# Performance work log

Measured on AMD Instinct MI355X. Metric: run time of the kernel, lower is better.

The kernel has to match this reference:

```python
import jax, jax.numpy as jnp
import numpy as np

B, S, H, E, V = 256, 512, 512, 128, 30000
RNN_IN = H + E + 1  # weighted context + id embedding + rate


def setup_inputs() -> dict:
    key = jax.random.key(0)
    ks = jax.random.split(key, 16)
    nrm = lambda k, shape, s=0.02: jax.random.normal(k, shape, dtype=jnp.float32) * s
    return {
        "input_id": jax.random.randint(ks[0], (B, 1), 0, V),
        "input_rate": jax.random.uniform(ks[1], (B, 1), dtype=jnp.float32),
        "hidden": nrm(ks[2], (1, B, H), 1.0),
        "encoder_outputs": nrm(ks[3], (S, B, H), 1.0),
        "attn_mask": jax.random.randint(ks[4], (B, S), 0, 2),
        "constraint_vec": (jax.random.uniform(ks[5], (B, V)) > 0.3).astype(jnp.float32),
        "emb_id": nrm(ks[6], (V, E)),
        "attn_w": nrm(ks[7], (2 * H, H)),
        "attn_b": jnp.zeros((H,), jnp.float32),
        "v_w": nrm(ks[8], (H,)),
        "w_ih": nrm(ks[9], (3 * H, RNN_IN)),
        "w_hh": nrm(ks[10], (3 * H, H)),
        "b_ih": jnp.zeros((3 * H,), jnp.float32),
        "b_hh": jnp.zeros((3 * H,), jnp.float32),
        "fc_id_w": nrm(ks[11], (H, V)),
        "fc_id_b": jnp.zeros((V,), jnp.float32),
        "tandem_w": nrm(ks[12], (E + H, H)),
        "tandem_b": jnp.zeros((H,), jnp.float32),
        "rate_w": nrm(ks[13], (H, 1)),
        "rate_b": jnp.zeros((1,), jnp.float32),
    }


def reference(input_id, input_rate, hidden, encoder_outputs, attn_mask,
              constraint_vec, emb_id, attn_w, attn_b, v_w,
              w_ih, w_hh, b_ih, b_hh, fc_id_w, fc_id_b,
              tandem_w, tandem_b, rate_w, rate_b):
    hd = hidden.shape[-1]
    h0 = hidden[0]                                # [B, H]
    embedded = emb_id[input_id[:, 0]]             # [B, E] (dropout p=0 -> identity)

    # --- additive attention (concat-linear split to avoid [B,S,2H] concat) ---
    enc = jnp.transpose(encoder_outputs, (1, 0, 2))         # [B, S, H]
    hid_part = h0 @ attn_w[:hd]                             # [B, H]
    enc_part = jnp.einsum('bsh,hk->bsk', enc, attn_w[hd:])  # [B, S, H]
    energy = jnp.tanh(hid_part[:, None, :] + enc_part + attn_b)
    scores = jnp.einsum('bsh,h->bs', energy, v_w)           # [B, S]
    scores = jnp.where(attn_mask == 0, jnp.float32(-1e10), scores)
    a = jax.nn.softmax(scores, axis=1)
    weighted = jnp.einsum('bs,bsh->bh', a, enc)             # [B, H]

    # --- GRU cell (torch gate order: r, z, n) ---
    x = jnp.concatenate([weighted, embedded, input_rate], axis=1)  # [B, H+E+1]
    gi = x @ w_ih.T + b_ih
    gh = h0 @ w_hh.T + b_hh
    gi_r, gi_z, gi_n = jnp.split(gi, 3, axis=1)
    gh_r, gh_z, gh_n = jnp.split(gh, 3, axis=1)
    r = jax.nn.sigmoid(gi_r + gh_r)
    z = jax.nn.sigmoid(gi_z + gh_z)
    n = jnp.tanh(gi_n + r * gh_n)
    h1 = (1.0 - z) * n + z * h0                   # [B, H]

    # --- masked log-softmax over id vocabulary ---
    logits = h1 @ fc_id_w + fc_id_b               # [B, V]
    maxes = jnp.max(logits, axis=1, keepdims=True)
    x_exp = jnp.exp(logits - maxes) * constraint_vec
    pred = jnp.clip(x_exp / jnp.sum(x_exp, axis=1, keepdims=True), 1e-6, 1.0)
    prediction_id = jnp.log(pred)

    # --- tandem rate head ---
    max_id = jnp.argmax(prediction_id, axis=1)
    id_emb = emb_id[max_id]                       # [B, E]
    rate_in = jax.nn.relu(jnp.concatenate([id_emb, h1], axis=1) @ tandem_w + tandem_b)
    prediction_rate = jax.nn.sigmoid(rate_in @ rate_w + rate_b)  # [B, 1]

    return prediction_id, prediction_rate, h1[None]  # hidden [1, B, H]
```

## Files before the change

### kernel.cpp

```cpp
#include <hip/hip_runtime.h>
#include <hip/hip_bf16.h>

#define B_ 256
#define S_ 512
#define H_ 512
#define E_ 128
#define V_ 30000
#define RNNIN_ 641

using bf16x8 = __attribute__((ext_vector_type(8))) short;
using f32x4  = __attribute__((ext_vector_type(4))) float;

__device__ __forceinline__ short f2bf(float f) {
  unsigned int u = __float_as_uint(f);
  u += 0x7fffu + ((u >> 16) & 1u);
  return (short)(u >> 16);
}

__device__ __forceinline__ float fast_tanh(float x) {
  x = fminf(10.f, fmaxf(-10.f, x));
  float t = __expf(2.f * x);
  return (t - 1.f) / (t + 1.f);
}

__device__ __forceinline__ float sigmoidf(float x) {
  return 1.f / (1.f + __expf(-x));
}

__global__ __launch_bounds__(256) void transpose_cvt(
    const float* __restrict__ in, unsigned short* __restrict__ out, int K, int N)
{
  __shared__ unsigned short tile[32][33];
  int n0 = blockIdx.x * 32, k0 = blockIdx.y * 32;
  int tx = threadIdx.x, ty = threadIdx.y;
  #pragma unroll
  for (int i = 0; i < 4; i++) {
    int k = k0 + ty + i * 8, n = n0 + tx;
    float v = (k < K && n < N) ? in[(size_t)k * N + n] : 0.f;
    tile[ty + i * 8][tx] = (unsigned short)f2bf(v);
  }
  __syncthreads();
  #pragma unroll
  for (int i = 0; i < 4; i++) {
    int n = n0 + ty + i * 8, k = k0 + tx;
    if (n < N && k < K) out[(size_t)n * K + k] = tile[tx][ty + i * 8];
  }
}

template<bool BT, bool RELU>
__global__ __launch_bounds__(256) void gemm_f32(
    const float* __restrict__ A, const float* __restrict__ Bm,
    const float* __restrict__ bias, float* __restrict__ C,
    int M, int N, int K)
{
  __shared__ float As[16][65];
  __shared__ float Bs[16][65];
  const int m0 = blockIdx.x * 64, n0 = blockIdx.y * 64;
  const int tid = threadIdx.x;
  const int tx = tid & 15, ty = tid >> 4;
  float acc[4][4] = {};
  for (int k0 = 0; k0 < K; k0 += 16) {
    __syncthreads();
    #pragma unroll
    for (int i = 0; i < 4; i++) {
      int e = tid + i * 256;
      int m = e >> 4, k = e & 15;
      float v = 0.f;
      if (m0 + m < M && k0 + k < K) v = A[(size_t)(m0 + m) * K + k0 + k];
      As[k][m] = v;
    }
    #pragma unroll
    for (int i = 0; i < 4; i++) {
      int e = tid + i * 256;
      if (BT) {
        int n = e >> 4, k = e & 15;
        float v = 0.f;
        if (n0 + n < N && k0 + k < K) v = Bm[(size_t)(n0 + n) * K + k0 + k];
        Bs[k][n] = v;
      } else {
        int k = e >> 6, n = e & 63;
        float v = 0.f;
        if (n0 + n < N && k0 + k < K) v = Bm[(size_t)(k0 + k) * N + n0 + n];
        Bs[k][n] = v;
      }
    }
    __syncthreads();
    #pragma unroll
    for (int k = 0; k < 16; k++) {
      float a[4], b[4];
      #pragma unroll
      for (int i = 0; i < 4; i++) a[i] = As[k][ty * 4 + i];
      #pragma unroll
      for (int j = 0; j < 4; j++) b[j] = Bs[k][tx * 4 + j];
      #pragma unroll
      for (int i = 0; i < 4; i++)
        #pragma unroll
        for (int j = 0; j < 4; j++) acc[i][j] += a[i] * b[j];
    }
  }
  #pragma unroll
  for (int i = 0; i < 4; i++) {
    int m = m0 + ty * 4 + i;
    if (m >= M) continue;
    #pragma unroll
    for (int j = 0; j < 4; j++) {
      int n = n0 + tx * 4 + j;
      if (n >= N) continue;
      float v = acc[i][j] + (bias ? bias[n] : 0.f);
      if (RELU) v = fmaxf(v, 0.f);
      C[(size_t)m * N + n] = v;
    }
  }
}

__global__ __launch_bounds__(512, 4) void attn_gemm_score(
    const float* __restrict__ A, const unsigned short* __restrict__ Bt,
    const float* __restrict__ hid_pb, const float* __restrict__ v_w,
    float* __restrict__ scores)
{
  __shared__ short As[4 * 64 * 8];
  __shared__ short Bs[8 * 4 * 64 * 8];
  const int m0 = blockIdx.x * 64;
  const int tid = threadIdx.x;
  const int lane = tid & 63;
  const int wv = tid >> 6;
  const int quad = lane >> 4, l15 = lane & 15;

  f32x4 acc[4][4];
  #pragma unroll
  for (int i = 0; i < 4; i++)
    #pragma unroll
    for (int j = 0; j < 4; j++) acc[i][j] = f32x4{0.f, 0.f, 0.f, 0.f};

  for (int kt = 0; kt < 16; kt++) {
    const int kb = kt * 32;
    __syncthreads();
    if (tid < 256) {
      int m = tid >> 2, q = tid & 3;
      const float* src = A + (size_t)(m0 + m) * H_ + kb + q * 8;
      float4 v0 = *(const float4*)src;
      float4 v1 = *(const float4*)(src + 4);
      bf16x8 pk;
      pk[0] = f2bf(v0.x); pk[1] = f2bf(v0.y); pk[2] = f2bf(v0.z); pk[3] = f2bf(v0.w);
      pk[4] = f2bf(v1.x); pk[5] = f2bf(v1.y); pk[6] = f2bf(v1.z); pk[7] = f2bf(v1.w);
      int ti = m >> 4, ld = q * 16 + (m & 15);
      *(bf16x8*)&As[(ti * 64 + ld) * 8] = pk;
    }
    #pragma unroll
    for (int p = 0; p < 4; p++) {
      int n = p * 128 + (tid >> 2), q = tid & 3;
      bf16x8 v = *(const bf16x8*)(Bt + (size_t)n * H_ + kb + q * 8);
      int wvd = n >> 6, tj = (n >> 4) & 3, ld = q * 16 + (n & 15);
      *(bf16x8*)&Bs[((wvd * 4 + tj) * 64 + ld) * 8] = v;
    }
    __syncthreads();
    bf16x8 a[4], b[4];
    #pragma unroll
    for (int ti = 0; ti < 4; ti++) a[ti] = *(const bf16x8*)&As[(ti * 64 + lane) * 8];
    #pragma unroll
    for (int tj = 0; tj < 4; tj++) b[tj] = *(const bf16x8*)&Bs[((wv * 4 + tj) * 64 + lane) * 8];
    #pragma unroll
    for (int ti = 0; ti < 4; ti++)
      #pragma unroll
      for (int tj = 0; tj < 4; tj++)
        acc[ti][tj] = __builtin_amdgcn_mfma_f32_16x16x32_bf16(a[ti], b[tj], acc[ti][tj], 0, 0, 0);
  }

  #pragma unroll
  for (int ti = 0; ti < 4; ti++) {
    #pragma unroll
    for (int r = 0; r < 4; r++) {
      int m = m0 + ti * 16 + quad * 4 + r;
      int b = m & (B_ - 1);
      int s = m >> 8;
      float sum = 0.f;
      #pragma unroll
      for (int tj = 0; tj < 4; tj++) {
        int n = wv * 64 + tj * 16 + l15;
        float v = acc[ti][tj][r] + hid_pb[b * H_ + n];
        sum += fast_tanh(v) * v_w[n];
      }
      sum += __shfl_xor(sum, 1);
      sum += __shfl_xor(sum, 2);
      sum += __shfl_xor(sum, 4);
      sum += __shfl_xor(sum, 8);
      if (l15 == 0) atomicAdd(scores + b * S_ + s, sum);
    }
  }
}

__global__ __launch_bounds__(256, 4) void logits_gemm(
    const unsigned short* __restrict__ Ab, const float* __restrict__ Bw,
    const float* __restrict__ bias, float* __restrict__ C)
{
  __shared__ short As[2 * 16 * 64 * 8];
  __shared__ short Bs[2 * 4 * 64 * 8];
  const int n0 = blockIdx.x * 64;
  const int tid = threadIdx.x;
  const int lane = tid & 63;
  const int wv = tid >> 6;
  const int quad = lane >> 4, l15 = lane & 15;

  f32x4 acc[4][4];
  #pragma unroll
  for (int i = 0; i < 4; i++)
    #pragma unroll
    for (int j = 0; j < 4; j++) acc[i][j] = f32x4{0.f, 0.f, 0.f, 0.f};

  const int nB  = tid & 63;
  const int kg  = tid >> 6;
  const int cB  = kg >> 1;
  const int q0  = (kg & 1) * 2;
  const int tjB = nB >> 4;
  const bool nOK = (n0 + nB) < V_;

  for (int kt = 0; kt < 8; kt++) {
    const int kb = kt * 64;
    __syncthreads();
    #pragma unroll
    for (int p = 0; p < 8; p++) {
      int m = p * 32 + (tid >> 3), f = tid & 7;
      int c = f >> 2, q = f & 3;
      bf16x8 v = *(const bf16x8*)(Ab + (size_t)m * H_ + kb + c * 32 + q * 8);
      int mt = m >> 4, ld = q * 16 + (m & 15);
      *(bf16x8*)&As[((c * 16 + mt) * 64 + ld) * 8] = v;
    }
    {
      float col[16];
      const float* src = Bw + (size_t)(kb + kg * 16) * V_ + n0 + nB;
      #pragma unroll
      for (int i = 0; i < 16; i++) col[i] = nOK ? src[(size_t)i * V_] : 0.f;
      bf16x8 f0, f1;
      #pragma unroll
      for (int i = 0; i < 8; i++) { f0[i] = f2bf(col[i]); f1[i] = f2bf(col[8 + i]); }
      int ld0 = q0 * 16 + (nB & 15);
      *(bf16x8*)&Bs[((cB * 4 + tjB) * 64 + ld0) * 8] = f0;
      *(bf16x8*)&Bs[((cB * 4 + tjB) * 64 + ld0 + 16) * 8] = f1;
    }
    __syncthreads();
    #pragma unroll
    for (int c = 0; c < 2; c++) {
      bf16x8 a[4], b[4];
      #pragma unroll
      for (int ti = 0; ti < 4; ti++)
        a[ti] = *(const bf16x8*)&As[((c * 16 + wv * 4 + ti) * 64 + lane) * 8];
      #pragma unroll
      for (int tj = 0; tj < 4; tj++)
        b[tj] = *(const bf16x8*)&Bs[((c * 4 + tj) * 64 + lane) * 8];
      #pragma unroll
      for (int ti = 0; ti < 4; ti++)
        #pragma unroll
        for (int tj = 0; tj < 4; tj++)
          acc[ti][tj] = __builtin_amdgcn_mfma_f32_16x16x32_bf16(a[ti], b[tj], acc[ti][tj], 0, 0, 0);
    }
  }
  #pragma unroll
  for (int ti = 0; ti < 4; ti++)
    #pragma unroll
    for (int r = 0; r < 4; r++) {
      int m = wv * 64 + ti * 16 + quad * 4 + r;
      #pragma unroll
      for (int tj = 0; tj < 4; tj++) {
        int n = n0 + tj * 16 + l15;
        if (n < V_) C[(size_t)m * V_ + n] = acc[ti][tj][r] + bias[n];
      }
    }
}

__global__ __launch_bounds__(256) void attn_softmax(
    const float* __restrict__ scores, const int* __restrict__ mask, float* __restrict__ aw)
{
  int b = blockIdx.x, tid = threadIdx.x;
  __shared__ float red[256];
  float v0 = scores[b * S_ + tid];
  float v1 = scores[b * S_ + tid + 256];
  if (mask[b * S_ + tid] == 0) v0 = -1e10f;
  if (mask[b * S_ + tid + 256] == 0) v1 = -1e10f;
  red[tid] = fmaxf(v0, v1);
  __syncthreads();
  for (int off = 128; off; off >>= 1) { if (tid < off) red[tid] = fmaxf(red[tid], red[tid + off]); __syncthreads(); }
  float mx = red[0];
  __syncthreads();
  float e0 = __expf(v0 - mx), e1 = __expf(v1 - mx);
  red[tid] = e0 + e1;
  __syncthreads();
  for (int off = 128; off; off >>= 1) { if (tid < off) red[tid] += red[tid + off]; __syncthreads(); }
  float inv = 1.f / red[0];
  aw[b * S_ + tid] = e0 * inv;
  aw[b * S_ + tid + 256] = e1 * inv;
}

__global__ __launch_bounds__(512) void attn_weighted(
    const float* __restrict__ aw, const float* __restrict__ enc, float* __restrict__ weighted)
{
  int b = blockIdx.x, h = threadIdx.x;
  __shared__ float a_s[S_];
  a_s[h] = aw[b * S_ + h];
  __syncthreads();
  float acc = 0.f;
  #pragma unroll 8
  for (int s = 0; s < S_; s++)
    acc += a_s[s] * enc[((size_t)s * B_ + b) * H_ + h];
  weighted[b * H_ + h] = acc;
}

__global__ void build_x(const float* __restrict__ weighted, const int* __restrict__ ids,
                        const float* __restrict__ emb, const float* __restrict__ rate,
                        float* __restrict__ x)
{
  int i = blockIdx.x * 256 + threadIdx.x;
  if (i >= B_ * RNNIN_) return;
  int b = i / RNNIN_, j = i % RNNIN_;
  float v;
  if (j < H_) v = weighted[b * H_ + j];
  else if (j < H_ + E_) v = emb[(size_t)ids[b] * E_ + (j - H_)];
  else v = rate[b];
  x[i] = v;
}

__global__ void gru_gates(const float* __restrict__ gi, const float* __restrict__ gh,
                          const float* __restrict__ h0, float* __restrict__ h1,
                          unsigned short* __restrict__ h1b, float* __restrict__ h1_out)
{
  int i = blockIdx.x * 256 + threadIdx.x;
  int b = i >> 9, j = i & (H_ - 1);
  const float* gib = gi + (size_t)b * 1536;
  const float* ghb = gh + (size_t)b * 1536;
  float r = sigmoidf(gib[j] + ghb[j]);
  float z = sigmoidf(gib[512 + j] + ghb[512 + j]);
  float n = fast_tanh(gib[1024 + j] + r * ghb[1024 + j]);
  float h = (1.f - z) * n + z * h0[i];
  h1[i] = h;
  h1b[i] = (unsigned short)f2bf(h);
  h1_out[i] = h;
}

__global__ __launch_bounds__(1024) void softmax_fused(
    float* __restrict__ lp, const float* __restrict__ cv, int* __restrict__ maxid)
{
  int b = blockIdx.x, tid = threadIdx.x;
  int wid = tid >> 6, lane = tid & 63;
  float* row = lp + (size_t)b * V_;
  const float* cvr = cv + (size_t)b * V_;
  __shared__ float redf[16];
  __shared__ float rede[16];
  __shared__ int   redi[16];

  float mx = -INFINITY;
  for (int v = tid; v < V_; v += 1024) mx = fmaxf(mx, row[v]);
  #pragma unroll
  for (int o = 1; o < 64; o <<= 1) mx = fmaxf(mx, __shfl_xor(mx, o));
  if (lane == 0) redf[wid] = mx;
  __syncthreads();
  if (tid == 0) {
    float m = redf[0];
    for (int i = 1; i < 16; i++) m = fmaxf(m, redf[i]);
    redf[0] = m;
  }
  __syncthreads();
  float M = redf[0];
  __syncthreads();

  float s = 0.f, best = -1.f;
  int bi = 0;
  for (int v = tid; v < V_; v += 1024) {
    float e = __expf(row[v] - M) * cvr[v];
    row[v] = e;
    s += e;
    if (e > best) { best = e; bi = v; }
  }
  #pragma unroll
  for (int o = 1; o < 64; o <<= 1) {
    s += __shfl_xor(s, o);
    float ob = __shfl_xor(best, o);
    int oi = __shfl_xor(bi, o);
    if (ob > best || (ob == best && oi < bi)) { best = ob; bi = oi; }
  }
  if (lane == 0) { redf[wid] = s; rede[wid] = best; redi[wid] = bi; }
  __syncthreads();
  if (tid == 0) {
    float ss = 0.f, bb = rede[0];
    int ii = redi[0];
    for (int i = 0; i < 16; i++) {
      ss += redf[i];
      if (rede[i] > bb || (rede[i] == bb && redi[i] < ii)) { bb = rede[i]; ii = redi[i]; }
    }
    redf[0] = ss;
    maxid[b] = ii;
  }
  __syncthreads();
  float inv = 1.f / redf[0];
  for (int v = tid; v < V_; v += 1024) {
    float p = row[v] * inv;
    p = fminf(fmaxf(p, 1e-6f), 1.f);
    row[v] = __logf(p);
  }
}

__global__ void build_tandem(const int* __restrict__ maxid, const float* __restrict__ emb,
                             const float* __restrict__ h1, float* __restrict__ t)
{
  int i = blockIdx.x * 256 + threadIdx.x;
  if (i >= B_ * 640) return;
  int b = i / 640, j = i % 640;
  t[i] = (j < E_) ? emb[(size_t)maxid[b] * E_ + j] : h1[b * H_ + (j - E_)];
}

__global__ __launch_bounds__(64) void rate_head(const float* __restrict__ rate_in,
                                                const float* __restrict__ rate_w,
                                                const float* __restrict__ rate_b,
                                                float* __restrict__ out)
{
  int b = blockIdx.x, t = threadIdx.x;
  float s = 0.f;
  #pragma unroll
  for (int i = 0; i < 8; i++) s += rate_in[b * H_ + t + 64 * i] * rate_w[t + 64 * i];
  #pragma unroll
  for (int m = 32; m; m >>= 1) s += __shfl_xor(s, m);
  if (t == 0) out[b] = sigmoidf(s + rate_b[0]);
}

extern "C" void kernel_launch(void* const* d_in, const int* in_sizes, int n_in,
                              void* d_out, int out_size, void* d_ws, size_t ws_size,
                              hipStream_t stream)
{
  const int*   input_id   = (const int*)  d_in[0];
  const float* input_rate = (const float*)d_in[1];
  const float* hidden     = (const float*)d_in[2];
  const float* enc        = (const float*)d_in[3];
  const int*   attn_mask  = (const int*)  d_in[4];
  const float* cv         = (const float*)d_in[5];
  const float* emb        = (const float*)d_in[6];
  const float* attn_w     = (const float*)d_in[7];
  const float* attn_b     = (const float*)d_in[8];
  const float* v_w        = (const float*)d_in[9];
  const float* w_ih       = (const float*)d_in[10];
  const float* w_hh       = (const float*)d_in[11];
  const float* b_ih       = (const float*)d_in[12];
  const float* b_hh       = (const float*)d_in[13];
  const float* fc_w       = (const float*)d_in[14];
  const float* fc_b       = (const float*)d_in[15];
  const float* tan_w      = (const float*)d_in[16];
  const float* tan_b      = (const float*)d_in[17];
  const float* rate_w     = (const float*)d_in[18];
  const float* rate_b     = (const float*)d_in[19];

  float* out = (float*)d_out;
  float* ws  = (float*)d_ws;
  float* hid_pb   = ws;
  float* scores   = ws + 131072;
  float* aw       = ws + 262144;
  float* weighted = ws + 393216;
  float* xbuf     = ws + 524288;
  float* gi       = ws + 688384;
  float* gh       = ws + 1081600;
  float* h1       = ws + 1474816;
  float* rate_in  = ws + 1605888;
  int*   maxid    = (int*)(ws + 1736960);
  unsigned short* Bt  = (unsigned short*)(ws + 1737216);
  unsigned short* h1b = (unsigned short*)(ws + 1868288);

  float* out_pred = out;
  float* out_rate = out + (size_t)B_ * V_;
  float* out_h1   = out + (size_t)B_ * V_ + B_;

  transpose_cvt<<<dim3(16, 16), dim3(32, 8), 0, stream>>>(attn_w + (size_t)H_ * H_, Bt, H_, H_);

  hipMemsetAsync(scores, 0, (size_t)B_ * S_ * sizeof(float), stream);

  gemm_f32<false, false><<<dim3(4, 8), 256, 0, stream>>>(hidden, attn_w, attn_b, hid_pb, B_, H_, H_);

  attn_gemm_score<<<2048, 512, 0, stream>>>(enc, Bt, hid_pb, v_w, scores);

  attn_softmax<<<B_, 256, 0, stream>>>(scores, attn_mask, aw);
  attn_weighted<<<B_, 512, 0, stream>>>(aw, enc, weighted);
  build_x<<<641, 256, 0, stream>>>(weighted, input_id, emb, input_rate, xbuf);

  gemm_f32<true, false><<<dim3(4, 24), 256, 0, stream>>>(xbuf, w_ih, b_ih, gi, B_, 1536, RNNIN_);
  gemm_f32<true, false><<<dim3(4, 24), 256, 0, stream>>>(hidden, w_hh, b_hh, gh, B_, 1536, H_);
  gru_gates<<<512, 256, 0, stream>>>(gi, gh, hidden, h1, h1b, out_h1);

  logits_gemm<<<469, 256, 0, stream>>>(h1b, fc_w, fc_b, out_pred);
  softmax_fused<<<B_, 1024, 0, stream>>>(out_pred, cv, maxid);

  build_tandem<<<640, 256, 0, stream>>>(maxid, emb, h1, xbuf);
  gemm_f32<false, true><<<dim3(4, 8), 256, 0, stream>>>(xbuf, tan_w, tan_b, rate_in, B_, H_, 640);
  rate_head<<<B_, 64, 0, stream>>>(rate_in, rate_w, rate_b, out_rate);
}
```

Before: 1.177 ms.

## Restructure attention score GEMM with direct-to-LDS B loads and register prefetch

Result: faster. 1.042 ms (-11.5%).

```diff
diff --git a/kernel.cpp b/kernel.cpp
--- a/kernel.cpp
+++ b/kernel.cpp
@@ -27,24 +27,20 @@
   return 1.f / (1.f + __expf(-x));
 }
 
-__global__ __launch_bounds__(256) void transpose_cvt(
-    const float* __restrict__ in, unsigned short* __restrict__ out, int K, int N)
-{
-  __shared__ unsigned short tile[32][33];
-  int n0 = blockIdx.x * 32, k0 = blockIdx.y * 32;
-  int tx = threadIdx.x, ty = threadIdx.y;
-  #pragma unroll
-  for (int i = 0; i < 4; i++) {
-    int k = k0 + ty + i * 8, n = n0 + tx;
-    float v = (k < K && n < N) ? in[(size_t)k * N + n] : 0.f;
-    tile[ty + i * 8][tx] = (unsigned short)f2bf(v);
-  }
-  __syncthreads();
-  #pragma unroll
-  for (int i = 0; i < 4; i++) {
-    int n = n0 + ty + i * 8, k = k0 + tx;
-    if (n < N && k < K) out[(size_t)n * K + k] = tile[tx][ty + i * 8];
-  }
+__device__ __forceinline__ void gload_lds16(const void* g, void* l) {
+  __builtin_amdgcn_global_load_lds(
+      (const __attribute__((address_space(1))) void*)g,
+      (__attribute__((address_space(3))) void*)l, 16, 0, 0);
+}
+
+__global__ __launch_bounds__(256) void pack_b(
+    const float* __restrict__ in, unsigned short* __restrict__ out)
+{
+  int i = blockIdx.x * 256 + threadIdx.x;
+  int k = i >> 9, n = i & 511;
+  float v = in[i];
+  int idx = ((((k >> 5) * 32 + (n >> 4)) * 4 + ((k >> 3) & 3)) * 16 + (n & 15)) * 8 + (k & 7);
+  out[idx] = (unsigned short)f2bf(v);
 }
 
 template<bool BT, bool RELU>
@@ -113,70 +109,171 @@
   }
 }
 
-__global__ __launch_bounds__(512, 4) void attn_gemm_score(
-    const float* __restrict__ A, const unsigned short* __restrict__ Bt,
+__device__ void gemm_bt_dev(float (*As)[65], float (*Bs)[65],
+    const float* __restrict__ A, const float* __restrict__ Bm,
+    const float* __restrict__ bias, float* __restrict__ C,
+    int M, int N, int K)
+{
+  const int m0 = blockIdx.x * 64, n0 = blockIdx.y * 64;
+  const int tid = threadIdx.x;
+  const int tx = tid & 15, ty = tid >> 4;
+  float acc[4][4] = {};
+  for (int k0 = 0; k0 < K; k0 += 16) {
+    __syncthreads();
+    #pragma unroll
+    for (int i = 0; i < 4; i++) {
+      int e = tid + i * 256;
+      int m = e >> 4, k = e & 15;
+      float v = 0.f;
+      if (m0 + m < M && k0 + k < K) v = A[(size_t)(m0 + m) * K + k0 + k];
+      As[k][m] = v;
+    }
+    #pragma unroll
+    for (int i = 0; i < 4; i++) {
+      int e = tid + i * 256;
+      int n = e >> 4, k = e & 15;
+      float v = 0.f;
+      if (n0 + n < N && k0 + k < K) v = Bm[(size_t)(n0 + n) * K + k0 + k];
+      Bs[k][n] = v;
+    }
+    __syncthreads();
+    #pragma unroll
+    for (int k = 0; k < 16; k++) {
+      float a[4], b[4];
+      #pragma unroll
+      for (int i = 0; i < 4; i++) a[i] = As[k][ty * 4 + i];
+      #pragma unroll
+      for (int j = 0; j < 4; j++) b[j] = Bs[k][tx * 4 + j];
+      #pragma unroll
+      for (int i = 0; i < 4; i++)
+        #pragma unroll
+        for (int j = 0; j < 4; j++) acc[i][j] += a[i] * b[j];
+    }
+  }
+  #pragma unroll
+  for (int i = 0; i < 4; i++) {
+    int m = m0 + ty * 4 + i;
+    if (m >= M) continue;
+    #pragma unroll
+    for (int j = 0; j < 4; j++) {
+      int n = n0 + tx * 4 + j;
+      if (n >= N) continue;
+      C[(size_t)m * N + n] = acc[i][j] + bias[n];
+    }
+  }
+}
+
+__global__ __launch_bounds__(256) void gemm_gru(
+    const float* __restrict__ xb, const float* __restrict__ w_ih,
+    const float* __restrict__ b_ih, float* __restrict__ gi,
+    const float* __restrict__ hid, const float* __restrict__ w_hh,
+    const float* __restrict__ b_hh, float* __restrict__ gh)
+{
+  __shared__ float As[16][65];
+  __shared__ float Bs[16][65];
+  if (blockIdx.z == 0) gemm_bt_dev(As, Bs, xb, w_ih, b_ih, gi, B_, 1536, RNNIN_);
+  else                 gemm_bt_dev(As, Bs, hid, w_hh, b_hh, gh, B_, 1536, H_);
+}
+
+__global__ __launch_bounds__(256, 3) void attn_gemm_score(
+    const float* __restrict__ A, const unsigned short* __restrict__ Btf,
     const float* __restrict__ hid_pb, const float* __restrict__ v_w,
     float* __restrict__ scores)
 {
-  __shared__ short As[4 * 64 * 8];
-  __shared__ short Bs[8 * 4 * 64 * 8];
-  const int m0 = blockIdx.x * 64;
-  const int tid = threadIdx.x;
+  __shared__ short As[2 * 4 * 64 * 8];
+  __shared__ short Bs[2 * 16 * 64 * 8];
+
+  const int bid  = blockIdx.x;
+  const int tile = (bid & 7) * 512 + (bid >> 3);
+  const int mblk = tile >> 1, nblk = tile & 1;
+  const int m0 = mblk * 64, n0 = nblk * 256;
+
+  const int tid  = threadIdx.x;
   const int lane = tid & 63;
-  const int wv = tid >> 6;
+  const int wv   = tid >> 6;
   const int quad = lane >> 4, l15 = lane & 15;
 
+  const int arow = tid >> 2;
+  const int aseg = tid & 3;
+  const float* aptr = A + (size_t)(m0 + arow) * H_ + aseg * 16;
+  const int ac = aseg >> 1, aq0 = (aseg & 1) * 2;
+  short* aw0 = &As[((ac * 4 + (arow >> 4)) * 64 + aq0 * 16 + (arow & 15)) * 8];
+  short* aw1 = aw0 + 16 * 8;
+
+  const unsigned short* bsrc = Btf + nblk * 8192;
+
   f32x4 acc[4][4];
   #pragma unroll
   for (int i = 0; i < 4; i++)
     #pragma unroll
     for (int j = 0; j < 4; j++) acc[i][j] = f32x4{0.f, 0.f, 0.f, 0.f};
 
-  for (int kt = 0; kt < 16; kt++) {
-    const int kb = kt * 32;
-    __syncthreads();
-    if (tid < 256) {
-      int m = tid >> 2, q = tid & 3;
-      const float* src = A + (size_t)(m0 + m) * H_ + kb + q * 8;
-      float4 v0 = *(const float4*)src;
-      float4 v1 = *(const float4*)(src + 4);
-      bf16x8 pk;
-      pk[0] = f2bf(v0.x); pk[1] = f2bf(v0.y); pk[2] = f2bf(v0.z); pk[3] = f2bf(v0.w);
-      pk[4] = f2bf(v1.x); pk[5] = f2bf(v1.y); pk[6] = f2bf(v1.z); pk[7] = f2bf(v1.w);
-      int ti = m >> 4, ld = q * 16 + (m & 15);
-      *(bf16x8*)&As[(ti * 64 + ld) * 8] = pk;
-    }
-    #pragma unroll
-    for (int p = 0; p < 4; p++) {
-      int n = p * 128 + (tid >> 2), q = tid & 3;
-      bf16x8 v = *(const bf16x8*)(Bt + (size_t)n * H_ + kb + q * 8);
-      int wvd = n >> 6, tj = (n >> 4) & 3, ld = q * 16 + (n & 15);
-      *(bf16x8*)&Bs[((wvd * 4 + tj) * 64 + ld) * 8] = v;
-    }
-    __syncthreads();
-    bf16x8 a[4], b[4];
-    #pragma unroll
-    for (int ti = 0; ti < 4; ti++) a[ti] = *(const bf16x8*)&As[(ti * 64 + lane) * 8];
-    #pragma unroll
-    for (int tj = 0; tj < 4; tj++) b[tj] = *(const bf16x8*)&Bs[((wv * 4 + tj) * 64 + lane) * 8];
-    #pragma unroll
-    for (int ti = 0; ti < 4; ti++)
+  float4 rA[4];
+  #pragma unroll
+  for (int i = 0; i < 4; i++) rA[i] = *(const float4*)(aptr + i * 4);
+
+  for (int kt = 0; kt < 8; kt++) {
+    __builtin_amdgcn_s_barrier();
+    asm volatile("s_waitcnt vmcnt(0)" ::: "memory");
+
+    #pragma unroll
+    for (int i = 0; i < 8; i++) {
+      const unsigned short* g = bsrc + (kt * 2 + (i >> 2)) * 16384
+                                     + ((i & 3) * 256 + tid) * 8;
+      gload_lds16((const void*)g, (void*)&Bs[(i * 256 + wv * 64) * 8]);
+    }
+
+    {
+      bf16x8 f0, f1;
+      f0[0] = f2bf(rA[0].x); f0[1] = f2bf(rA[0].y); f0[2] = f2bf(rA[0].z); f0[3] = f2bf(rA[0].w);
+      f0[4] = f2bf(rA[1].x); f0[5] = f2bf(rA[1].y); f0[6] = f2bf(rA[1].z); f0[7] = f2bf(rA[1].w);
+      f1[0] = f2bf(rA[2].x); f1[1] = f2bf(rA[2].y); f1[2] = f2bf(rA[2].z); f1[3] = f2bf(rA[2].w);
+      f1[4] = f2bf(rA[3].x); f1[5] = f2bf(rA[3].y); f1[6] = f2bf(rA[3].z); f1[7] = f2bf(rA[3].w);
+      *(bf16x8*)aw0 = f0;
+      *(bf16x8*)aw1 = f1;
+    }
+
+    if (kt < 7) {
+      asm volatile("" ::: "memory");
+      const float* anext = aptr + (kt + 1) * 64;
+      #pragma unroll
+      for (int i = 0; i < 4; i++) rA[i] = *(const float4*)(anext + i * 4);
+      asm volatile("s_waitcnt vmcnt(4) lgkmcnt(0)" ::: "memory");
+    } else {
+      asm volatile("s_waitcnt vmcnt(0) lgkmcnt(0)" ::: "memory");
+    }
+    __builtin_amdgcn_s_barrier();
+    asm volatile("" ::: "memory");
+
+    #pragma unroll
+    for (int ch = 0; ch < 2; ch++) {
+      bf16x8 a[4], b[4];
+      #pragma unroll
+      for (int ti = 0; ti < 4; ti++)
+        a[ti] = *(const bf16x8*)&As[((ch * 4 + ti) * 64 + lane) * 8];
       #pragma unroll
       for (int tj = 0; tj < 4; tj++)
-        acc[ti][tj] = __builtin_amdgcn_mfma_f32_16x16x32_bf16(a[ti], b[tj], acc[ti][tj], 0, 0, 0);
-  }
-
+        b[tj] = *(const bf16x8*)&Bs[((ch * 16 + wv * 4 + tj) * 64 + lane) * 8];
+      #pragma unroll
+      for (int ti = 0; ti < 4; ti++)
+        #pragma unroll
+        for (int tj = 0; tj < 4; tj++)
+          acc[ti][tj] = __builtin_amdgcn_mfma_f32_16x16x32_bf16(a[ti], b[tj], acc[ti][tj], 0, 0, 0);
+    }
+  }
+
+  __syncthreads();
+  float* part = (float*)As;
   #pragma unroll
   for (int ti = 0; ti < 4; ti++) {
     #pragma unroll
     for (int r = 0; r < 4; r++) {
       int m = m0 + ti * 16 + quad * 4 + r;
       int b = m & (B_ - 1);
-      int s = m >> 8;
       float sum = 0.f;
       #pragma unroll
       for (int tj = 0; tj < 4; tj++) {
-        int n = wv * 64 + tj * 16 + l15;
+        int n = n0 + wv * 64 + tj * 16 + l15;
         float v = acc[ti][tj][r] + hid_pb[b * H_ + n];
         sum += fast_tanh(v) * v_w[n];
       }
@@ -184,8 +281,14 @@
       sum += __shfl_xor(sum, 2);
       sum += __shfl_xor(sum, 4);
       sum += __shfl_xor(sum, 8);
-      if (l15 == 0) atomicAdd(scores + b * S_ + s, sum);
-    }
+      if (l15 == 0) part[(ti * 16 + quad * 4 + r) * 4 + wv] = sum;
+    }
+  }
+  __syncthreads();
+  if (tid < 64) {
+    float s4 = part[tid * 4 + 0] + part[tid * 4 + 1] + part[tid * 4 + 2] + part[tid * 4 + 3];
+    int m = m0 + tid;
+    atomicAdd(scores + (m & (B_ - 1)) * S_ + (m >> 8), s4);
   }
 }
 
@@ -290,21 +393,22 @@
   aw[b * S_ + tid + 256] = e1 * inv;
 }
 
-__global__ __launch_bounds__(512) void attn_weighted(
-    const float* __restrict__ aw, const float* __restrict__ enc, float* __restrict__ weighted)
-{
-  int b = blockIdx.x, h = threadIdx.x;
-  __shared__ float a_s[S_];
-  a_s[h] = aw[b * S_ + h];
-  __syncthreads();
+__global__ __launch_bounds__(512) void attn_weighted_part(
+    const float* __restrict__ aw, const float* __restrict__ enc, float* __restrict__ wpart)
+{
+  int b = blockIdx.x, c = blockIdx.y, h = threadIdx.x;
+  __shared__ float a_s[128];
+  if (h < 128) a_s[h] = aw[b * S_ + c * 128 + h];
+  __syncthreads();
+  const float* ep = enc + ((size_t)(c * 128) * B_ + b) * H_ + h;
   float acc = 0.f;
   #pragma unroll 8
-  for (int s = 0; s < S_; s++)
-    acc += a_s[s] * enc[((size_t)s * B_ + b) * H_ + h];
-  weighted[b * H_ + h] = acc;
-}
-
-__global__ void build_x(const float* __restrict__ weighted, const int* __restrict__ ids,
+  for (int s = 0; s < 128; s++)
+    acc += a_s[s] * ep[(size_t)s * B_ * H_];
+  wpart[((size_t)c * B_ + b) * H_ + h] = acc;
+}
+
+__global__ void build_x(const float* __restrict__ wpart, const int* __restrict__ ids,
                         const float* __restrict__ emb, const float* __restrict__ rate,
                         float* __restrict__ x)
 {
@@ -312,7 +416,11 @@
   if (i >= B_ * RNNIN_) return;
   int b = i / RNNIN_, j = i % RNNIN_;
   float v;
-  if (j < H_) v = weighted[b * H_ + j];
+  if (j < H_) {
+    size_t o = (size_t)b * H_ + j;
+    const size_t st = (size_t)B_ * H_;
+    v = wpart[o] + wpart[o + st] + wpart[o + 2 * st] + wpart[o + 3 * st];
+  }
   else if (j < H_ + E_) v = emb[(size_t)ids[b] * E_ + (j - H_)];
   else v = rate[b];
   x[i] = v;
@@ -457,27 +565,28 @@
   float* h1       = ws + 1474816;
   float* rate_in  = ws + 1605888;
   int*   maxid    = (int*)(ws + 1736960);
-  unsigned short* Bt  = (unsigned short*)(ws + 1737216);
+  unsigned short* Btf = (unsigned short*)(ws + 1737216);
   unsigned short* h1b = (unsigned short*)(ws + 1868288);
+  float* wpart = gi;
 
   float* out_pred = out;
   float* out_rate = out + (size_t)B_ * V_;
   float* out_h1   = out + (size_t)B_ * V_ + B_;
-
-  transpose_cvt<<<dim3(16, 16), dim3(32, 8), 0, stream>>>(attn_w + (size_t)H_ * H_, Bt, H_, H_);
+  (void)weighted;
+
+  pack_b<<<1024, 256, 0, stream>>>(attn_w + (size_t)H_ * H_, Btf);
 
   hipMemsetAsync(scores, 0, (size_t)B_ * S_ * sizeof(float), stream);
 
   gemm_f32<false, false><<<dim3(4, 8), 256, 0, stream>>>(hidden, attn_w, attn_b, hid_pb, B_, H_, H_);
 
-  attn_gemm_score<<<2048, 512, 0, stream>>>(enc, Bt, hid_pb, v_w, scores);
+  attn_gemm_score<<<4096, 256, 0, stream>>>(enc, Btf, hid_pb, v_w, scores);
 
   attn_softmax<<<B_, 256, 0, stream>>>(scores, attn_mask, aw);
-  attn_weighted<<<B_, 512, 0, stream>>>(aw, enc, weighted);
-  build_x<<<641, 256, 0, stream>>>(weighted, input_id, emb, input_rate, xbuf);
-
-  gemm_f32<true, false><<<dim3(4, 24), 256, 0, stream>>>(xbuf, w_ih, b_ih, gi, B_, 1536, RNNIN_);
-  gemm_f32<true, false><<<dim3(4, 24), 256, 0, stream>>>(hidden, w_hh, b_hh, gh, B_, 1536, H_);
+  attn_weighted_part<<<dim3(B_, 4), 512, 0, stream>>>(aw, enc, wpart);
+  build_x<<<641, 256, 0, stream>>>(wpart, input_id, emb, input_rate, xbuf);
+
+  gemm_gru<<<dim3(4, 24, 2), 256, 0, stream>>>(xbuf, w_ih, b_ih, gi, hidden, w_hh, b_hh, gh);
   gru_gates<<<512, 256, 0, stream>>>(gi, gh, hidden, h1, h1b, out_h1);
 
   logits_gemm<<<469, 256, 0, stream>>>(h1b, fc_w, fc_b, out_pred);
```
